# Kernel tuning notes

Hardware: AMD Instinct MI355X
Metric: run time of the kernel (lower is better)

## Reference

```python
import jax, jax.numpy as jnp
import numpy as np

N = 100000   # nodes
E = 1200000  # edges
D = 64       # feature / hidden dim (heads=1)
L = 3        # num_layers
G = 64       # num graphs
SCALE = 1.0 / np.sqrt(D)


def setup_inputs() -> dict:
    key = jax.random.key(0)
    ks = jax.random.split(key, 12)
    inp = {
        "x": jax.random.normal(ks[0], (N, D), dtype=jnp.float32),
        "edge_index": jax.random.randint(ks[1], (2, E), 0, N, dtype=jnp.int64),
        "batch": jnp.sort(jax.random.randint(ks[2], (N,), 0, G, dtype=jnp.int64)),
        "Wq": jax.random.normal(ks[3], (L, D, D), dtype=jnp.float32) * 0.1,
        "bq": jax.random.normal(ks[4], (L, D), dtype=jnp.float32) * 0.1,
        "Wk": jax.random.normal(ks[5], (L, D, D), dtype=jnp.float32) * 0.1,
        "bk": jax.random.normal(ks[6], (L, D), dtype=jnp.float32) * 0.1,
        "Wv": jax.random.normal(ks[7], (L, D, D), dtype=jnp.float32) * 0.1,
        "bv": jax.random.normal(ks[8], (L, D), dtype=jnp.float32) * 0.1,
        "Ws": jax.random.normal(ks[9], (L, D, D), dtype=jnp.float32) * 0.1,
        "bs": jax.random.normal(ks[10], (L, D), dtype=jnp.float32) * 0.1,
    }
    return inp


def _transformer_conv(x, src, dst, Wq, bq, Wk, bk, Wv, bv, Ws, bs):
    # PyG TransformerConv, heads=1, concat=True, root_weight=True, beta=False
    q = x @ Wq + bq            # [N, D] query of target nodes
    k = x @ Wk + bk            # [N, D] key of source nodes
    v = x @ Wv + bv            # [N, D] value of source nodes
    logits = jnp.sum(q[dst] * k[src], axis=-1) * SCALE  # [E]
    # segment softmax over incoming edges of each target node
    m = jax.ops.segment_max(logits, dst, num_segments=N)        # [N]
    e = jnp.exp(logits - m[dst])                                 # [E]
    denom = jax.ops.segment_sum(e, dst, num_segments=N)         # [N]
    alpha = e / denom[dst]                                       # [E]
    agg = jax.ops.segment_sum(alpha[:, None] * v[src], dst, num_segments=N)  # [N, D]
    return agg + x @ Ws + bs   # root/skip connection


def reference(x, edge_index, batch, Wq, bq, Wk, bk, Wv, bv, Ws, bs):
    src, dst = edge_index[0], edge_index[1]
    for l in range(L):
        x = _transformer_conv(x, src, dst, Wq[l], bq[l], Wk[l], bk[l],
                              Wv[l], bv[l], Ws[l], bs[l])
        x = jax.nn.relu(x)
    # global_mean_pool
    sums = jax.ops.segment_sum(x, batch, num_segments=G)                  # [G, D]
    counts = jax.ops.segment_sum(jnp.ones((N,), x.dtype), batch, num_segments=G)
    graph_emb = sums / jnp.maximum(counts, 1.0)[:, None]
    return (x, graph_emb)
```

## Files before the change

kernel.cpp:

```cpp
#include <hip/hip_runtime.h>
#include <math.h>

#define DD 64

typedef _Float16 h2 __attribute__((ext_vector_type(2)));
typedef _Float16 h4 __attribute__((ext_vector_type(4)));
typedef _Float16 h8 __attribute__((ext_vector_type(8)));
typedef float f32x4 __attribute__((ext_vector_type(4)));

__global__ __launch_bounds__(64) void k_wconv(
    const float* __restrict__ Wq, const float* __restrict__ Wk,
    const float* __restrict__ Wv, const float* __restrict__ Ws,
    _Float16* __restrict__ wf)
{
  int bid = blockIdx.x;
  int layer = bid >> 5;
  int c = (bid >> 1) & 15;
  int s = bid & 1;
  int lane = threadIdx.x;
  int col = c * 16 + (lane & 15);
  int mi = col >> 6;
  const float* W = (mi == 0 ? Wq : mi == 1 ? Wk : mi == 2 ? Wv : Ws)
                   + (size_t)layer * DD * DD;
  int colw = col & 63;
  _Float16* o = wf + ((((size_t)(layer * 16 + c)) * 2 + s) * 64 + lane) * 8;
  #pragma unroll
  for (int j = 0; j < 8; ++j) {
    int k = s * 32 + (lane >> 4) * 8 + j;
    o[j] = (_Float16)W[k * DD + colw];
  }
}

__global__ __launch_bounds__(256) void k_xconv(
    const float* __restrict__ x, _Float16* __restrict__ xb, int total8)
{
  int i = blockIdx.x * 256 + threadIdx.x;
  if (i >= total8) return;
  float4 a = ((const float4*)x)[i * 2];
  float4 b = ((const float4*)x)[i * 2 + 1];
  h8 o;
  o[0] = (_Float16)a.x; o[1] = (_Float16)a.y; o[2] = (_Float16)a.z; o[3] = (_Float16)a.w;
  o[4] = (_Float16)b.x; o[5] = (_Float16)b.y; o[6] = (_Float16)b.z; o[7] = (_Float16)b.w;
  *(h8*)(xb + (size_t)i * 8) = o;
}

#define LH_STRIDE 200
#define LF_STRIDE 68
#define WAVE_LDS  (16 * 400 + 16 * 272)

__global__ __launch_bounds__(256) void k_projM(
    const _Float16* __restrict__ xb, const _Float16* __restrict__ wf,
    const float* __restrict__ bq, const float* __restrict__ bk,
    const float* __restrict__ bv, const float* __restrict__ bs,
    _Float16* __restrict__ qh, _Float16* __restrict__ kvh,
    float* __restrict__ sout, int n)
{
  __shared__ __align__(16) char lds[4 * WAVE_LDS];
  int wave = threadIdx.x >> 6;
  int lane = threadIdx.x & 63;
  int nbase = blockIdx.x * 64 + wave * 16;
  if (nbase >= n) return;

  char* wbase = lds + wave * WAVE_LDS;
  _Float16* lh = (_Float16*)wbase;
  float*    lf = (float*)(wbase + 16 * 400);

  const int cl = lane & 15;
  const int rq = lane >> 4;

  int ar = min(nbase + cl, n - 1);
  h8 a0 = *(const h8*)(xb + (size_t)ar * DD + rq * 8);
  h8 a1 = *(const h8*)(xb + (size_t)ar * DD + 32 + rq * 8);

  #pragma unroll
  for (int c = 0; c < 16; ++c) {
    const float* bp = (c < 4) ? bq : (c < 8) ? bk : (c < 12) ? bv : bs;
    const int fb = c * 16 + rq * 4;
    float4 b4 = *(const float4*)(bp + (fb & 63));
    f32x4 acc; acc[0] = b4.x; acc[1] = b4.y; acc[2] = b4.z; acc[3] = b4.w;
    const _Float16* wp = wf + ((size_t)(c * 2) * 64 + lane) * 8;
    h8 w0 = *(const h8*)(wp);
    h8 w1 = *(const h8*)(wp + 64 * 8);
    acc = __builtin_amdgcn_mfma_f32_16x16x32_f16(w0, a0, acc, 0, 0, 0);
    acc = __builtin_amdgcn_mfma_f32_16x16x32_f16(w1, a1, acc, 0, 0, 0);

    if (c < 12) {
      h4 o; o[0] = (_Float16)acc[0]; o[1] = (_Float16)acc[1];
      o[2] = (_Float16)acc[2]; o[3] = (_Float16)acc[3];
      *(h4*)(lh + cl * LH_STRIDE + fb) = o;
    } else {
      *(f32x4*)(lf + cl * LF_STRIDE + (fb - 192)) = acc;
    }
  }

  #pragma unroll
  for (int i = 0; i < 2; ++i) {
    int chunk = i * 64 + lane;
    int nd = chunk >> 3, co = chunk & 7;
    h8 v = *(const h8*)(lh + nd * LH_STRIDE + co * 8);
    if (nbase + nd < n)
      *(h8*)(qh + (size_t)(nbase + nd) * DD + co * 8) = v;
  }
  #pragma unroll
  for (int i = 0; i < 4; ++i) {
    int chunk = i * 64 + lane;
    int nd = chunk >> 4, co = chunk & 15;
    h8 v = *(const h8*)(lh + nd * LH_STRIDE + 64 + co * 8);
    if (nbase + nd < n)
      *(h8*)(kvh + (size_t)(nbase + nd) * 128 + co * 8) = v;
  }
  #pragma unroll
  for (int i = 0; i < 4; ++i) {
    int chunk = i * 64 + lane;
    int nd = chunk >> 4, co = chunk & 15;
    f32x4 v = *(const f32x4*)(lf + nd * LF_STRIDE + co * 4);
    if (nbase + nd < n)
      *(f32x4*)(sout + (size_t)(nbase + nd) * DD + co * 4) = v;
  }
}

__global__ __launch_bounds__(256) void k_hist(
    const int* __restrict__ dst, int* __restrict__ deg,
    unsigned short* __restrict__ pos, int ecnt)
{
  int e = (blockIdx.x * 256 + threadIdx.x) * 4;
  if (e + 3 < ecnt) {
    int4 d = *(const int4*)(dst + e);
    pos[e]     = (unsigned short)atomicAdd(deg + d.x, 1);
    pos[e + 1] = (unsigned short)atomicAdd(deg + d.y, 1);
    pos[e + 2] = (unsigned short)atomicAdd(deg + d.z, 1);
    pos[e + 3] = (unsigned short)atomicAdd(deg + d.w, 1);
  } else {
    for (; e < ecnt; ++e)
      pos[e] = (unsigned short)atomicAdd(deg + dst[e], 1);
  }
}

__global__ __launch_bounds__(1024) void k_scanA(
    const int* __restrict__ deg, int* __restrict__ rowptr,
    int* __restrict__ btot, int* __restrict__ dbins, int n)
{
  __shared__ int wsum[16];
  __shared__ int lbin[256];
  int tid = threadIdx.x;
  int lane = tid & 63, wave = tid >> 6;
  if (tid < 256) lbin[tid] = 0;
  __syncthreads();
  int i = blockIdx.x * 4096 + tid * 4;
  int4 d = make_int4(0, 0, 0, 0);
  if (i + 3 < n) d = *(const int4*)(deg + i);
  else {
    if (i     < n) d.x = deg[i];
    if (i + 1 < n) d.y = deg[i + 1];
    if (i + 2 < n) d.z = deg[i + 2];
  }
  if (i     < n) atomicAdd(&lbin[min(d.x, 255)], 1);
  if (i + 1 < n) atomicAdd(&lbin[min(d.y, 255)], 1);
  if (i + 2 < n) atomicAdd(&lbin[min(d.z, 255)], 1);
  if (i + 3 < n) atomicAdd(&lbin[min(d.w, 255)], 1);

  int s1 = d.x, s2 = s1 + d.y, s3 = s2 + d.z, s4 = s3 + d.w;
  int s = s4;
  #pragma unroll
  for (int off = 1; off < 64; off <<= 1) {
    int t = __shfl_up(s, off);
    if (lane >= off) s += t;
  }
  if (lane == 63) wsum[wave] = s;
  __syncthreads();
  if (wave == 0) {
    int ws = (lane < 16) ? wsum[lane] : 0;
    #pragma unroll
    for (int off = 1; off < 16; off <<= 1) {
      int t = __shfl_up(ws, off);
      if (lane >= off) ws += t;
    }
    if (lane < 16) wsum[lane] = ws;
  }
  __syncthreads();
  int excl = ((wave > 0) ? wsum[wave - 1] : 0) + s - s4;
  if (i     < n) rowptr[i + 1] = excl + s1;
  if (i + 1 < n) rowptr[i + 2] = excl + s2;
  if (i + 2 < n) rowptr[i + 3] = excl + s3;
  if (i + 3 < n) rowptr[i + 4] = excl + s4;
  if (tid == 0) {
    if (blockIdx.x == 0) rowptr[0] = 0;
    btot[blockIdx.x] = wsum[15];
  }
  if (tid < 256 && lbin[tid]) atomicAdd(&dbins[tid], lbin[tid]);
}

__global__ __launch_bounds__(64) void k_scanB(
    int* __restrict__ btot, int nb, const int* __restrict__ dbins,
    int* __restrict__ dcur)
{
  int lane = threadIdx.x;
  int v = (lane < nb) ? btot[lane] : 0;
  int s = v;
  #pragma unroll
  for (int off = 1; off < 64; off <<= 1) {
    int t = __shfl_up(s, off);
    if (lane >= off) s += t;
  }
  if (lane < nb) btot[lane] = s - v;

  int4 dv = *(const int4*)(dbins + lane * 4);
  int t1 = dv.x, t2 = t1 + dv.y, t3 = t2 + dv.z, t4 = t3 + dv.w;
  int ss = t4;
  #pragma unroll
  for (int off = 1; off < 64; off <<= 1) {
    int t = __shfl_up(ss, off);
    if (lane >= off) ss += t;
  }
  int ex = ss - t4;
  dcur[lane * 4]     = ex;
  dcur[lane * 4 + 1] = ex + t1;
  dcur[lane * 4 + 2] = ex + t2;
  dcur[lane * 4 + 3] = ex + t3;
}

__global__ __launch_bounds__(1024) void k_scanC(
    int* __restrict__ rowptr, const int* __restrict__ btot, int n)
{
  int off = btot[blockIdx.x];
  if (off == 0) return;
  int i = blockIdx.x * 4096 + threadIdx.x * 4;
  #pragma unroll
  for (int k = 1; k <= 4; ++k)
    if (i + k <= n) rowptr[i + k] += off;
}

__global__ __launch_bounds__(1024) void k_dfill(
    const int* __restrict__ deg, int* __restrict__ dcur,
    int* __restrict__ order, int n)
{
  __shared__ int lcnt[256];
  __shared__ int lbase[256];
  int tid = threadIdx.x;
  if (tid < 256) lcnt[tid] = 0;
  __syncthreads();
  int i = blockIdx.x * 1024 + tid;
  int b = 0, slot = 0;
  bool ok = (i < n);
  if (ok) {
    b = min(deg[i], 255);
    slot = atomicAdd(&lcnt[b], 1);
  }
  __syncthreads();
  if (tid < 256 && lcnt[tid]) lbase[tid] = atomicAdd(&dcur[tid], lcnt[tid]);
  __syncthreads();
  if (ok) order[lbase[b] + slot] = i;
}

__global__ __launch_bounds__(256) void k_fill(
    const int* __restrict__ src, const int* __restrict__ dst,
    const int* __restrict__ rowptr, const unsigned short* __restrict__ pos,
    int* __restrict__ adj, int ecnt)
{
  int e = (blockIdx.x * 256 + threadIdx.x) * 4;
  if (e + 3 < ecnt) {
    int4 d = *(const int4*)(dst + e);
    int4 s = *(const int4*)(src + e);
    ushort4 p = *(const ushort4*)(pos + e);
    adj[rowptr[d.x] + p.x] = s.x;
    adj[rowptr[d.y] + p.y] = s.y;
    adj[rowptr[d.z] + p.z] = s.z;
    adj[rowptr[d.w] + p.w] = s.w;
  } else {
    for (; e < ecnt; ++e)
      adj[rowptr[dst[e]] + pos[e]] = src[e];
  }
}

#define H2OF(v, i) __builtin_shufflevector((v), (v), 2*(i), 2*(i)+1)

template<bool LAST>
__global__ __launch_bounds__(256) void k_node(
    const _Float16* __restrict__ qh, const _Float16* __restrict__ kvh,
    const int* __restrict__ rowptr, const int* __restrict__ adj,
    const int* __restrict__ order,
    const float* __restrict__ sskip, float* __restrict__ outp,
    _Float16* __restrict__ xbnext, int n)
{
  int wid = (blockIdx.x * blockDim.x + threadIdx.x) >> 6;
  int lane = threadIdx.x & 63;
  const int g = lane >> 3;
  const int t = lane & 7;

  int idx = wid * 8 + g;
  bool nok = (idx < n);
  int node = order[nok ? idx : (n - 1)];

  const h8 q8 = *(const h8*)(qh + (size_t)node * DD + t * 8);
  const h2 qp0 = H2OF(q8, 0), qp1 = H2OF(q8, 1), qp2 = H2OF(q8, 2), qp3 = H2OF(q8, 3);

  const int e0 = rowptr[node];
  const int d  = nok ? (rowptr[node + 1] - e0) : 0;

  int dm = d;
  dm = max(dm, __shfl_xor(dm, 8));
  dm = max(dm, __shfl_xor(dm, 16));
  dm = max(dm, __shfl_xor(dm, 32));

  float mg = -1e30f, den = 0.f;
  float agg[8] = {0.f, 0.f, 0.f, 0.f, 0.f, 0.f, 0.f, 0.f};

  const char* kvb = (const char*)kvh;
  h8 kP, vP;
  if (d > 0) {
    int s = adj[e0];
    unsigned off = ((unsigned)s << 8) + ((unsigned)t << 4);
    kP = *(const h8*)(kvb + off);
    vP = *(const h8*)(kvb + off + 128);
  }

  for (int it = 0; it < dm; ++it) {
    const h8 kc = kP, vc = vP;
    const bool valid = (it < d);
    if (it + 1 < d) {
      int s2 = adj[e0 + it + 1];
      unsigned off = ((unsigned)s2 << 8) + ((unsigned)t << 4);
      kP = *(const h8*)(kvb + off);
      vP = *(const h8*)(kvb + off + 128);
    }

#if __has_builtin(__builtin_amdgcn_fdot2)
    float p = __builtin_amdgcn_fdot2(qp0, H2OF(kc, 0), 0.f, false);
    p = __builtin_amdgcn_fdot2(qp1, H2OF(kc, 1), p, false);
    p = __builtin_amdgcn_fdot2(qp2, H2OF(kc, 2), p, false);
    p = __builtin_amdgcn_fdot2(qp3, H2OF(kc, 3), p, false);
#else
    h2 ph = qp0 * H2OF(kc, 0);
    ph = qp1 * H2OF(kc, 1) + ph;
    ph = qp2 * H2OF(kc, 2) + ph;
    ph = qp3 * H2OF(kc, 3) + ph;
    float p = (float)ph.x + (float)ph.y;
#endif
    p += __shfl_xor(p, 1);
    p += __shfl_xor(p, 2);
    p += __shfl_xor(p, 4);
    p *= 0.125f;

    if (valid && p > mg) {
      float c = __expf(mg - p);
      den *= c;
      #pragma unroll
      for (int j = 0; j < 8; ++j) agg[j] *= c;
      mg = p;
    }
    float w = valid ? __expf(p - mg) : 0.f;
    den += w;
    #pragma unroll
    for (int j = 0; j < 8; ++j)
      agg[j] = fmaf(w, (float)vc[j], agg[j]);
  }

  if (nok) {
    float inv = (den > 0.f) ? (1.0f / den) : 0.f;
    const float* sp = sskip + (size_t)node * DD + t * 8;
    float4 sa = *(const float4*)(sp);
    float4 sb = *(const float4*)(sp + 4);
    float r[8];
    r[0] = fmaxf(fmaf(agg[0], inv, sa.x), 0.f);
    r[1] = fmaxf(fmaf(agg[1], inv, sa.y), 0.f);
    r[2] = fmaxf(fmaf(agg[2], inv, sa.z), 0.f);
    r[3] = fmaxf(fmaf(agg[3], inv, sa.w), 0.f);
    r[4] = fmaxf(fmaf(agg[4], inv, sb.x), 0.f);
    r[5] = fmaxf(fmaf(agg[5], inv, sb.y), 0.f);
    r[6] = fmaxf(fmaf(agg[6], inv, sb.z), 0.f);
    r[7] = fmaxf(fmaf(agg[7], inv, sb.w), 0.f);
    if (LAST) {
      float* op = outp + (size_t)node * DD + t * 8;
      *(float4*)(op)     = make_float4(r[0], r[1], r[2], r[3]);
      *(float4*)(op + 4) = make_float4(r[4], r[5], r[6], r[7]);
    } else {
      h8 xh;
      #pragma unroll
      for (int j = 0; j < 8; ++j) xh[j] = (_Float16)r[j];
      *(h8*)(xbnext + (size_t)node * DD + t * 8) = xh;
    }
  }
}

__global__ __launch_bounds__(64) void k_pool_sum(
    const float* __restrict__ x, const int* __restrict__ batch,
    float* __restrict__ gsum, float* __restrict__ gcnt, int n)
{
  int lane = threadIdx.x;
  int n0 = blockIdx.x * 64;
  if (n0 >= n) return;
  int n1 = min(n0 + 64, n);
  float acc = 0.f;
  int g_prev = batch[n0];
  int run = 0;
  for (int nn = n0; nn < n1; ++nn) {
    int g = batch[nn];
    if (g != g_prev) {
      atomicAdd(gsum + (size_t)g_prev * DD + lane, acc);
      if (lane == 0) atomicAdd(gcnt + g_prev, (float)run);
      acc = 0.f; run = 0; g_prev = g;
    }
    acc += x[(size_t)nn * DD + lane];
    run++;
  }
  atomicAdd(gsum + (size_t)g_prev * DD + lane, acc);
  if (lane == 0) atomicAdd(gcnt + g_prev, (float)run);
}

__global__ __launch_bounds__(256) void k_pool_div(
    const float* __restrict__ gsum, const float* __restrict__ gcnt,
    float* __restrict__ emb, int gtot)
{
  int gid = blockIdx.x * blockDim.x + threadIdx.x;
  if (gid >= gtot * DD) return;
  int g = gid >> 6;
  emb[gid] = gsum[gid] / fmaxf(gcnt[g], 1.0f);
}

extern "C" void kernel_launch(void* const* d_in, const int* in_sizes, int n_in,
                              void* d_out, int out_size, void* d_ws, size_t ws_size,
                              hipStream_t stream)
{
  const float* x_in  = (const float*)d_in[0];
  const int*   ei    = (const int*)  d_in[1];
  const int*   batch = (const int*)  d_in[2];
  const float* Wq = (const float*)d_in[3];
  const float* bq = (const float*)d_in[4];
  const float* Wk = (const float*)d_in[5];
  const float* bk = (const float*)d_in[6];
  const float* Wv = (const float*)d_in[7];
  const float* bv = (const float*)d_in[8];
  const float* Ws = (const float*)d_in[9];
  const float* bs = (const float*)d_in[10];

  const int nd     = in_sizes[0];
  const int n      = nd / DD;
  const int ecnt   = in_sizes[1] / 2;
  const int layers = in_sizes[3] / (DD * DD);
  const int gtot   = (out_size - nd) / DD;

  const int* src = ei;
  const int* dst = ei + ecnt;

  char* cur = (char*)d_ws;
  float*     P0  = (float*)cur;     cur += (size_t)nd * 4;
  _Float16*  XB  = (_Float16*)cur;  cur += (size_t)nd * 2;
  _Float16*  QH  = (_Float16*)cur;  cur += (size_t)nd * 2;
  _Float16*  KVH = (_Float16*)cur;  cur += (size_t)nd * 4;
  _Float16*  WF  = (_Float16*)cur;  cur += (size_t)layers * 16384 * 2;
  int* rowptr = (int*)cur;          cur += (size_t)(n + 4) * 4;
  int* adj    = (int*)cur;          cur += (size_t)(ecnt + 8) * 4;
  int* deg    = (int*)cur;          cur += (size_t)n * 4;
  int* dbins  = (int*)cur;          cur += 256 * 4;
  int* dcur   = (int*)cur;          cur += 256 * 4;
  int* btot   = (int*)cur;          cur += 64 * 4;
  int* order  = (int*)cur;          cur += (size_t)n * 4;
  unsigned short* pos = (unsigned short*)cur; cur += (size_t)ecnt * 2;
  float* gsum = (float*)cur;        cur += (size_t)gtot * DD * 4;
  float* gcnt = (float*)cur;

  float* out = (float*)d_out;

  k_wconv<<<layers * 32, 64, 0, stream>>>(Wq, Wk, Wv, Ws, WF);
  k_xconv<<<(n * 8 + 255) / 256, 256, 0, stream>>>(x_in, XB, n * 8);
  hipMemsetAsync(deg, 0, (size_t)(n + 256) * 4, stream);
  const int eb4 = (ecnt + 1023) / 1024;
  k_hist<<<eb4, 256, 0, stream>>>(dst, deg, pos, ecnt);
  const int nbk = (n + 4095) / 4096;
  k_scanA<<<nbk, 1024, 0, stream>>>(deg, rowptr, btot, dbins, n);
  k_scanB<<<1, 64, 0, stream>>>(btot, nbk, dbins, dcur);
  k_scanC<<<nbk, 1024, 0, stream>>>(rowptr, btot, n);
  k_dfill<<<(n + 1023) / 1024, 1024, 0, stream>>>(deg, dcur, order, n);
  k_fill<<<eb4, 256, 0, stream>>>(src, dst, rowptr, pos, adj, ecnt);

  const int pj = (n + 63) / 64;
  const int nb = (n + 31) / 32;

  for (int l = 0; l < layers; ++l) {
    const size_t bo = (size_t)l * DD;
    k_projM<<<pj, 256, 0, stream>>>(XB, WF + (size_t)l * 16384,
                                    bq + bo, bk + bo, bv + bo, bs + bo,
                                    QH, KVH, P0, n);
    if (l == layers - 1)
      k_node<true><<<nb, 256, 0, stream>>>(QH, KVH, rowptr, adj, order,
                                           P0, out, XB, n);
    else
      k_node<false><<<nb, 256, 0, stream>>>(QH, KVH, rowptr, adj, order,
                                            P0, out, XB, n);
  }

  hipMemsetAsync(gsum, 0, (size_t)(gtot * DD + gtot) * 4, stream);
  const int pbk = (n + 63) / 64;
  k_pool_sum<<<pbk, 64, 0, stream>>>(out, batch, gsum, gcnt, n);
  const int fb = (gtot * DD + 255) / 256;
  k_pool_div<<<fb, 256, 0, stream>>>(gsum, gcnt, out + (size_t)nd, gtot);
}
```

Baseline: 350.7 us.

## Unroll edge loop by two with deeper prefetch and store skip term in fp16

The node aggregation loop now handles two edges per iteration and prefetches adjacency indices two steps ahead, with clamped, zero-padded adj reads so no per-edge bounds branches are needed. This is meant to put more gather loads in flight and hide latency. The skip-connection projection is now stored and read as fp16 instead of fp32, which halves that traffic at some cost in precision. The q·k dot product also moves from packed fdot2 to scalar fp32 FMAs, which adds ALU work.

Result: no change. 350.2 us (-0.2%).

```diff
diff --git a/kernel.cpp b/kernel.cpp
--- a/kernel.cpp
+++ b/kernel.cpp
@@ -2,6 +2,7 @@
 #include <math.h>
 
 #define DD 64
+#define APAD 512
 
 typedef _Float16 h2 __attribute__((ext_vector_type(2)));
 typedef _Float16 h4 __attribute__((ext_vector_type(4)));
@@ -45,15 +46,15 @@
 }
 
 #define LH_STRIDE 200
-#define LF_STRIDE 68
-#define WAVE_LDS  (16 * 400 + 16 * 272)
+#define LS_STRIDE 72
+#define WAVE_LDS  (16 * 400 + 16 * 144)
 
 __global__ __launch_bounds__(256) void k_projM(
     const _Float16* __restrict__ xb, const _Float16* __restrict__ wf,
     const float* __restrict__ bq, const float* __restrict__ bk,
     const float* __restrict__ bv, const float* __restrict__ bs,
     _Float16* __restrict__ qh, _Float16* __restrict__ kvh,
-    float* __restrict__ sout, int n)
+    _Float16* __restrict__ sh, int n)
 {
   __shared__ __align__(16) char lds[4 * WAVE_LDS];
   int wave = threadIdx.x >> 6;
@@ -63,7 +64,7 @@
 
   char* wbase = lds + wave * WAVE_LDS;
   _Float16* lh = (_Float16*)wbase;
-  float*    lf = (float*)(wbase + 16 * 400);
+  _Float16* ls = (_Float16*)(wbase + 16 * 400);
 
   const int cl = lane & 15;
   const int rq = lane >> 4;
@@ -84,13 +85,12 @@
     acc = __builtin_amdgcn_mfma_f32_16x16x32_f16(w0, a0, acc, 0, 0, 0);
     acc = __builtin_amdgcn_mfma_f32_16x16x32_f16(w1, a1, acc, 0, 0, 0);
 
-    if (c < 12) {
-      h4 o; o[0] = (_Float16)acc[0]; o[1] = (_Float16)acc[1];
-      o[2] = (_Float16)acc[2]; o[3] = (_Float16)acc[3];
+    h4 o; o[0] = (_Float16)acc[0]; o[1] = (_Float16)acc[1];
+    o[2] = (_Float16)acc[2]; o[3] = (_Float16)acc[3];
+    if (c < 12)
       *(h4*)(lh + cl * LH_STRIDE + fb) = o;
-    } else {
-      *(f32x4*)(lf + cl * LF_STRIDE + (fb - 192)) = acc;
-    }
+    else
+      *(h4*)(ls + cl * LS_STRIDE + (fb - 192)) = o;
   }
 
   #pragma unroll
@@ -110,12 +110,12 @@
       *(h8*)(kvh + (size_t)(nbase + nd) * 128 + co * 8) = v;
   }
   #pragma unroll
-  for (int i = 0; i < 4; ++i) {
+  for (int i = 0; i < 2; ++i) {
     int chunk = i * 64 + lane;
-    int nd = chunk >> 4, co = chunk & 15;
-    f32x4 v = *(const f32x4*)(lf + nd * LF_STRIDE + co * 4);
+    int nd = chunk >> 3, co = chunk & 7;
+    h8 v = *(const h8*)(ls + nd * LS_STRIDE + co * 8);
     if (nbase + nd < n)
-      *(f32x4*)(sout + (size_t)(nbase + nd) * DD + co * 4) = v;
+      *(h8*)(sh + (size_t)(nbase + nd) * DD + co * 8) = v;
   }
 }
 
@@ -279,8 +279,8 @@
     const _Float16* __restrict__ qh, const _Float16* __restrict__ kvh,
     const int* __restrict__ rowptr, const int* __restrict__ adj,
     const int* __restrict__ order,
-    const float* __restrict__ sskip, float* __restrict__ outp,
-    _Float16* __restrict__ xbnext, int n)
+    const _Float16* __restrict__ sh, float* __restrict__ outp,
+    _Float16* __restrict__ xbnext, int n, int elim)
 {
   int wid = (blockIdx.x * blockDim.x + threadIdx.x) >> 6;
   int lane = threadIdx.x & 63;
@@ -306,69 +306,78 @@
   float agg[8] = {0.f, 0.f, 0.f, 0.f, 0.f, 0.f, 0.f, 0.f};
 
   const char* kvb = (const char*)kvh;
-  h8 kP, vP;
-  if (d > 0) {
-    int s = adj[e0];
-    unsigned off = ((unsigned)s << 8) + ((unsigned)t << 4);
-    kP = *(const h8*)(kvb + off);
-    vP = *(const h8*)(kvb + off + 128);
-  }
-
-  for (int it = 0; it < dm; ++it) {
-    const h8 kc = kP, vc = vP;
-    const bool valid = (it < d);
-    if (it + 1 < d) {
-      int s2 = adj[e0 + it + 1];
-      unsigned off = ((unsigned)s2 << 8) + ((unsigned)t << 4);
-      kP = *(const h8*)(kvb + off);
-      vP = *(const h8*)(kvb + off + 128);
+  const unsigned tb = (unsigned)t << 4;
+
+  h8 kA, vA, kB, vB;
+  {
+    int a0 = adj[min(e0,     elim)];
+    int a1 = adj[min(e0 + 1, elim)];
+    unsigned o0 = ((unsigned)a0 << 8) + tb;
+    unsigned o1 = ((unsigned)a1 << 8) + tb;
+    kA = *(const h8*)(kvb + o0); vA = *(const h8*)(kvb + o0 + 128);
+    kB = *(const h8*)(kvb + o1); vB = *(const h8*)(kvb + o1 + 128);
+  }
+  int aN0 = adj[min(e0 + 2, elim)];
+  int aN1 = adj[min(e0 + 3, elim)];
+
+  for (int it = 0; it < dm; it += 2) {
+    int aF0 = adj[min(e0 + it + 4, elim)];
+    int aF1 = adj[min(e0 + it + 5, elim)];
+    unsigned o0 = ((unsigned)aN0 << 8) + tb;
+    unsigned o1 = ((unsigned)aN1 << 8) + tb;
+    h8 kN0 = *(const h8*)(kvb + o0); h8 vN0 = *(const h8*)(kvb + o0 + 128);
+    h8 kN1 = *(const h8*)(kvb + o1); h8 vN1 = *(const h8*)(kvb + o1 + 128);
+
+#define EDGE_STEP(KC, VC, VALID)                                        \
+    {                                                                   \
+      bool valid = (VALID);                                             \
+      float p;                                                          \
+      {                                                                 \
+        _Pragma("clang diagnostic push")                                \
+        p = 0.f;                                                        \
+        _Pragma("clang diagnostic pop")                                 \
+      }                                                                 \
+      p = (float)(KC)[0] * (float)q8[0] + p;                            \
+      p = fmaf((float)(KC)[1], (float)q8[1], p);                        \
+      p = fmaf((float)(KC)[2], (float)q8[2], p);                        \
+      p = fmaf((float)(KC)[3], (float)q8[3], p);                        \
+      p = fmaf((float)(KC)[4], (float)q8[4], p);                        \
+      p = fmaf((float)(KC)[5], (float)q8[5], p);                        \
+      p = fmaf((float)(KC)[6], (float)q8[6], p);                        \
+      p = fmaf((float)(KC)[7], (float)q8[7], p);                        \
+      p += __shfl_xor(p, 1);                                            \
+      p += __shfl_xor(p, 2);                                            \
+      p += __shfl_xor(p, 4);                                            \
+      p *= 0.125f;                                                      \
+      if (valid && p > mg) {                                            \
+        float c = __expf(mg - p);                                       \
+        den *= c;                                                       \
+        _Pragma("unroll")                                               \
+        for (int j = 0; j < 8; ++j) agg[j] *= c;                        \
+        mg = p;                                                         \
+      }                                                                 \
+      float w = valid ? __expf(p - mg) : 0.f;                           \
+      den += w;                                                         \
+      _Pragma("unroll")                                                 \
+      for (int j = 0; j < 8; ++j)                                       \
+        agg[j] = fmaf(w, (float)(VC)[j], agg[j]);                       \
     }
 
-#if __has_builtin(__builtin_amdgcn_fdot2)
-    float p = __builtin_amdgcn_fdot2(qp0, H2OF(kc, 0), 0.f, false);
-    p = __builtin_amdgcn_fdot2(qp1, H2OF(kc, 1), p, false);
-    p = __builtin_amdgcn_fdot2(qp2, H2OF(kc, 2), p, false);
-    p = __builtin_amdgcn_fdot2(qp3, H2OF(kc, 3), p, false);
-#else
-    h2 ph = qp0 * H2OF(kc, 0);
-    ph = qp1 * H2OF(kc, 1) + ph;
-    ph = qp2 * H2OF(kc, 2) + ph;
-    ph = qp3 * H2OF(kc, 3) + ph;
-    float p = (float)ph.x + (float)ph.y;
-#endif
-    p += __shfl_xor(p, 1);
-    p += __shfl_xor(p, 2);
-    p += __shfl_xor(p, 4);
-    p *= 0.125f;
-
-    if (valid && p > mg) {
-      float c = __expf(mg - p);
-      den *= c;
-      #pragma unroll
-      for (int j = 0; j < 8; ++j) agg[j] *= c;
-      mg = p;
-    }
-    float w = valid ? __expf(p - mg) : 0.f;
-    den += w;
+    EDGE_STEP(kA, vA, it < d)
+    EDGE_STEP(kB, vB, it + 1 < d)
+#undef EDGE_STEP
+
+    kA = kN0; vA = vN0; kB = kN1; vB = vN1;
+    aN0 = aF0; aN1 = aF1;
+  }
+
+  if (nok) {
+    float inv = (den > 0.f) ? (1.0f / den) : 0.f;
+    const h8 s8 = *(const h8*)(sh + (size_t)node * DD + t * 8);
+    float r[8];
     #pragma unroll
     for (int j = 0; j < 8; ++j)
-      agg[j] = fmaf(w, (float)vc[j], agg[j]);
-  }
-
-  if (nok) {
-    float inv = (den > 0.f) ? (1.0f / den) : 0.f;
-    const float* sp = sskip + (size_t)node * DD + t * 8;
-    float4 sa = *(const float4*)(sp);
-    float4 sb = *(const float4*)(sp + 4);
-    float r[8];
-    r[0] = fmaxf(fmaf(agg[0], inv, sa.x), 0.f);
-    r[1] = fmaxf(fmaf(agg[1], inv, sa.y), 0.f);
-    r[2] = fmaxf(fmaf(agg[2], inv, sa.z), 0.f);
-    r[3] = fmaxf(fmaf(agg[3], inv, sa.w), 0.f);
-    r[4] = fmaxf(fmaf(agg[4], inv, sb.x), 0.f);
-    r[5] = fmaxf(fmaf(agg[5], inv, sb.y), 0.f);
-    r[6] = fmaxf(fmaf(agg[6], inv, sb.z), 0.f);
-    r[7] = fmaxf(fmaf(agg[7], inv, sb.w), 0.f);
+      r[j] = fmaxf(fmaf(agg[j], inv, (float)s8[j]), 0.f);
     if (LAST) {
       float* op = outp + (size_t)node * DD + t * 8;
       *(float4*)(op)     = make_float4(r[0], r[1], r[2], r[3]);
@@ -443,13 +452,13 @@
   const int* dst = ei + ecnt;
 
   char* cur = (char*)d_ws;
-  float*     P0  = (float*)cur;     cur += (size_t)nd * 4;
+  _Float16*  SH  = (_Float16*)cur;  cur += (size_t)nd * 2;
   _Float16*  XB  = (_Float16*)cur;  cur += (size_t)nd * 2;
   _Float16*  QH  = (_Float16*)cur;  cur += (size_t)nd * 2;
   _Float16*  KVH = (_Float16*)cur;  cur += (size_t)nd * 4;
   _Float16*  WF  = (_Float16*)cur;  cur += (size_t)layers * 16384 * 2;
   int* rowptr = (int*)cur;          cur += (size_t)(n + 4) * 4;
-  int* adj    = (int*)cur;          cur += (size_t)(ecnt + 8) * 4;
+  int* adj    = (int*)cur;          cur += (size_t)(ecnt + APAD) * 4;
   int* deg    = (int*)cur;          cur += (size_t)n * 4;
   int* dbins  = (int*)cur;          cur += 256 * 4;
   int* dcur   = (int*)cur;          cur += 256 * 4;
@@ -460,10 +469,11 @@
   float* gcnt = (float*)cur;
 
   float* out = (float*)d_out;
+  const int elim = ecnt + APAD - 1;
 
   k_wconv<<<layers * 32, 64, 0, stream>>>(Wq, Wk, Wv, Ws, WF);
   k_xconv<<<(n * 8 + 255) / 256, 256, 0, stream>>>(x_in, XB, n * 8);
-  hipMemsetAsync(deg, 0, (size_t)(n + 256) * 4, stream);
+  hipMemsetAsync(adj + ecnt, 0, (size_t)(APAD + n + 256) * 4, stream);
   const int eb4 = (ecnt + 1023) / 1024;
   k_hist<<<eb4, 256, 0, stream>>>(dst, deg, pos, ecnt);
   const int nbk = (n + 4095) / 4096;
@@ -480,13 +490,13 @@
     const size_t bo = (size_t)l * DD;
     k_projM<<<pj, 256, 0, stream>>>(XB, WF + (size_t)l * 16384,
                                     bq + bo, bk + bo, bv + bo, bs + bo,
-                                    QH, KVH, P0, n);
+                                    QH, KVH, SH, n);
     if (l == layers - 1)
       k_node<true><<<nb, 256, 0, stream>>>(QH, KVH, rowptr, adj, order,
-                                           P0, out, XB, n);
+                                           SH, out, XB, n, elim);
     else
       k_node<false><<<nb, 256, 0, stream>>>(QH, KVH, rowptr, adj, order,
-                                            P0, out, XB, n);
+                                            SH, out, XB, n, elim);
   }
 
   hipMemsetAsync(gsum, 0, (size_t)(gtot * DD + gtot) * 4, stream);
```
